# Kernel tuning notes

Measured on AMD Instinct MI355X. Metric: run time of the kernel, lower is better.

Reference implementation:

```python
import jax, jax.numpy as jnp
import numpy as np

B, L = 2, 4096
D_MODEL, STATE, CONV, EXPAND, HEADDIM = 1024, 128, 4, 2, 64
D_INNER = EXPAND * D_MODEL            # 2048
NHEADS = D_INNER // HEADDIM           # 32
CONV_DIM = D_INNER + 2 * STATE        # x, B, C channels (ngroups=1)
D_IN_PROJ = 2 * D_INNER + 2 * STATE + NHEADS
MLP_INNER = 4096
EPS = 1e-5

def _silu(x):
    return x * jax.nn.sigmoid(x)

def _rmsnorm_prenorm(x, res, w):
    # rmsnorm_fn(prenorm=True): residual update then RMSNorm of the residual
    res = x + res
    normed = res * jax.lax.rsqrt(jnp.mean(res * res, axis=-1, keepdims=True) + EPS)
    return normed * w, res

def _mamba2(x, in_proj_w, conv_w, conv_b, dt_bias, A_log, D_param, out_proj_w):
    b, l, _ = x.shape
    zxbcdt = x @ in_proj_w.T                                   # (b,l,D_IN_PROJ)
    z, xBC, dt = jnp.split(zxbcdt, [D_INNER, D_INNER + CONV_DIM], axis=-1)
    # causal depthwise conv1d + silu over [x, B, C]
    xp = jnp.pad(xBC, ((0, 0), (CONV - 1, 0), (0, 0)))
    conv = sum(xp[:, j:j + l, :] * conv_w[None, None, :, j] for j in range(CONV)) + conv_b
    xBC = _silu(conv)
    xh, Bm, Cm = jnp.split(xBC, [D_INNER, D_INNER + STATE], axis=-1)
    xh = xh.reshape(b, l, NHEADS, HEADDIM)                     # (b,l,h,p)
    dt = jax.nn.softplus(dt + dt_bias)                         # (b,l,h)
    A = -jnp.exp(A_log)                                        # (h,)

    def step(state, inp):
        x_t, B_t, C_t, dt_t = inp                              # (b,h,p),(b,n),(b,n),(b,h)
        dA = jnp.exp(dt_t * A)                                 # (b,h)
        state = state * dA[..., None, None] + jnp.einsum('bh,bhp,bn->bhpn', dt_t, x_t, B_t)
        y_t = jnp.einsum('bhpn,bn->bhp', state, C_t)
        return state, y_t

    xs = (xh.transpose(1, 0, 2, 3), Bm.transpose(1, 0, 2), Cm.transpose(1, 0, 2), dt.transpose(1, 0, 2))
    state0 = jnp.zeros((b, NHEADS, HEADDIM, STATE), dtype=x.dtype)
    _, y = jax.lax.scan(step, state0, xs)                      # y: (l,b,h,p)
    y = y.transpose(1, 0, 2, 3) + D_param[None, None, :, None] * xh
    y = y * _silu(z).reshape(b, l, NHEADS, HEADDIM)            # rmsnorm=False -> gate with silu(z)
    return y.reshape(b, l, D_INNER) @ out_proj_w.T

def _mlp(x, gate_w, up_w, down_w):
    return (_silu(x @ gate_w.T) * (x @ up_w.T)) @ down_w.T

def setup_inputs() -> dict:
    key = jax.random.key(0)
    ks = jax.random.split(key, 12)
    s = 0.02
    return {
        'hidden_states': jax.random.normal(ks[0], (B, L, D_MODEL), jnp.float32),
        'residual': jax.random.normal(ks[1], (B, L, D_MODEL), jnp.float32),
        'ssm_norm_w': jnp.ones((D_MODEL,), jnp.float32),
        'mlp_norm_w': jnp.ones((D_MODEL,), jnp.float32),
        'in_proj_w': jax.random.normal(ks[2], (D_IN_PROJ, D_MODEL), jnp.float32) * s,
        'conv_w': jax.random.normal(ks[3], (CONV_DIM, CONV), jnp.float32) * 0.1,
        'conv_b': jnp.zeros((CONV_DIM,), jnp.float32),
        'dt_bias': jax.random.uniform(ks[4], (NHEADS,), jnp.float32, -4.0, -1.0),
        'A_log': jnp.log(jax.random.uniform(ks[5], (NHEADS,), jnp.float32, 1.0, 16.0)),
        'D_param': jnp.ones((NHEADS,), jnp.float32),
        'out_proj_w': jax.random.normal(ks[6], (D_MODEL, D_INNER), jnp.float32) * s,
        'mlp_gate_w': jax.random.normal(ks[7], (MLP_INNER, D_MODEL), jnp.float32) * s,
        'mlp_up_w': jax.random.normal(ks[8], (MLP_INNER, D_MODEL), jnp.float32) * s,
        'mlp_down_w': jax.random.normal(ks[9], (D_MODEL, MLP_INNER), jnp.float32) * s,
    }

def reference(hidden_states, residual, ssm_norm_w, mlp_norm_w, in_proj_w, conv_w, conv_b,
              dt_bias, A_log, D_param, out_proj_w, mlp_gate_w, mlp_up_w, mlp_down_w):
    h, res = _rmsnorm_prenorm(hidden_states, residual, ssm_norm_w)
    h = _mamba2(h, in_proj_w, conv_w, conv_b, dt_bias, A_log, D_param, out_proj_w)
    h, res = _rmsnorm_prenorm(h, res, mlp_norm_w)
    h = _mlp(h, mlp_gate_w, mlp_up_w, mlp_down_w)
    return h, res
```

## Files before the change

### kernel.cpp

```cpp
#include <hip/hip_runtime.h>

typedef __bf16 bf16x8 __attribute__((ext_vector_type(8)));
typedef float  f32x4  __attribute__((ext_vector_type(4)));

#define GLOAD_LDS16(gp, lp) \
  __builtin_amdgcn_global_load_lds((const __attribute__((address_space(1))) void*)(gp), \
                                   (__attribute__((address_space(3))) void*)(lp), 16, 0, 0)

__device__ __forceinline__ unsigned short f2bf(float f) {
  unsigned u = __float_as_uint(f);
  u += 0x7fffu + ((u >> 16) & 1u);
  return (unsigned short)(u >> 16);
}
__device__ __forceinline__ float bf2f(unsigned short h) {
  return __uint_as_float(((unsigned)h) << 16);
}
__device__ __forceinline__ f32x4 splat4(float v) { f32x4 r = {v, v, v, v}; return r; }

__device__ __forceinline__ f32x4 up4(unsigned lo, unsigned hi) {
  f32x4 r;
  r[0] = __uint_as_float(lo << 16); r[1] = __uint_as_float(lo & 0xffff0000u);
  r[2] = __uint_as_float(hi << 16); r[3] = __uint_as_float(hi & 0xffff0000u);
  return r;
}
__device__ __forceinline__ unsigned pk2(float a, float b) {
  return (unsigned)f2bf(a) | ((unsigned)f2bf(b) << 16);
}

__device__ __forceinline__ void store_out(unsigned short* C, size_t idx, float v) {
  C[idx] = f2bf(v);
}
__device__ __forceinline__ void store_out(float* C, size_t idx, float v) {
  C[idx] = v;
}

__global__ __launch_bounds__(256) void rmsnorm1_kernel(
    const float* __restrict__ hid, const float* __restrict__ resin,
    const float* __restrict__ w, float* __restrict__ resout,
    unsigned short* __restrict__ hout)
{
  const int row = blockIdx.x, t = threadIdx.x;
  const size_t base = (size_t)row * 1024;
  float4 h = ((const float4*)(hid + base))[t];
  float4 r = ((const float4*)(resin + base))[t];
  float4 s; s.x = h.x + r.x; s.y = h.y + r.y; s.z = h.z + r.z; s.w = h.w + r.w;
  float ss = s.x*s.x + s.y*s.y + s.z*s.z + s.w*s.w;
  #pragma unroll
  for (int off = 32; off; off >>= 1) ss += __shfl_down(ss, off, 64);
  __shared__ float red[4];
  if ((t & 63) == 0) red[t >> 6] = ss;
  __syncthreads();
  float tot = red[0] + red[1] + red[2] + red[3];
  float sc = rsqrtf(tot * (1.0f/1024.0f) + 1e-5f);
  ((float4*)(resout + base))[t] = s;
  float4 wv = ((const float4*)w)[t];
  ushort4 o = make_ushort4(f2bf(s.x*sc*wv.x), f2bf(s.y*sc*wv.y),
                           f2bf(s.z*sc*wv.z), f2bf(s.w*sc*wv.w));
  ((ushort4*)(hout + base))[t] = o;
}

__global__ __launch_bounds__(256) void rmsnorm2_kernel(
    const unsigned short* __restrict__ mo, const float* __restrict__ res1,
    const float* __restrict__ w, float* __restrict__ res_out,
    unsigned short* __restrict__ h2)
{
  const int row = blockIdx.x, t = threadIdx.x;
  const size_t base = (size_t)row * 1024;
  float4 r = ((const float4*)(res1 + base))[t];
  ushort4 m = ((const ushort4*)(mo + base))[t];
  float4 s; s.x = r.x + bf2f(m.x); s.y = r.y + bf2f(m.y);
            s.z = r.z + bf2f(m.z); s.w = r.w + bf2f(m.w);
  float ss = s.x*s.x + s.y*s.y + s.z*s.z + s.w*s.w;
  #pragma unroll
  for (int off = 32; off; off >>= 1) ss += __shfl_down(ss, off, 64);
  __shared__ float red[4];
  if ((t & 63) == 0) red[t >> 6] = ss;
  __syncthreads();
  float tot = red[0] + red[1] + red[2] + red[3];
  float sc = rsqrtf(tot * (1.0f/1024.0f) + 1e-5f);
  ((float4*)(res_out + base))[t] = s;
  float4 wv = ((const float4*)w)[t];
  ((ushort4*)(h2 + base))[t] = make_ushort4(f2bf(s.x*sc*wv.x), f2bf(s.y*sc*wv.y),
                                            f2bf(s.z*sc*wv.z), f2bf(s.w*sc*wv.w));
}

__global__ __launch_bounds__(256) void cast_w(
    const float* __restrict__ src, unsigned short* __restrict__ dst,
    int rows, int cols, int prows)
{
  size_t i4 = ((size_t)blockIdx.x * 256 + threadIdx.x) * 4;
  size_t total = (size_t)prows * cols;
  if (i4 >= total) return;
  int r = (int)(i4 / cols);
  ushort4 o;
  if (r < rows) {
    float4 v = *(const float4*)(src + i4);
    o = make_ushort4(f2bf(v.x), f2bf(v.y), f2bf(v.z), f2bf(v.w));
  } else {
    o = make_ushort4(0, 0, 0, 0);
  }
  *(ushort4*)(dst + i4) = o;
}

template <typename OutT>
__global__ __launch_bounds__(256) void gemm_bt(
    const unsigned short* __restrict__ A, const unsigned short* __restrict__ W,
    OutT* __restrict__ C, int M, int N, int K, int lda, int ldc)
{
  __shared__ unsigned short As[128 * 32];
  __shared__ unsigned short Bs[128 * 32];
  const int tid = threadIdx.x;
  const int wave = tid >> 6, lane = tid & 63;
  const int m0 = blockIdx.y << 7, n0 = blockIdx.x << 7;
  const int lr = lane >> 2;
  const int lk = (lane & 3) << 3;
  const int wm = (wave >> 1) << 6, wn = (wave & 1) << 6;
  const int fr = lane & 15, fq = lane >> 4;

  f32x4 acc[4][4];
  #pragma unroll
  for (int i = 0; i < 4; i++)
    #pragma unroll
    for (int j = 0; j < 4; j++)
      #pragma unroll
      for (int r = 0; r < 4; r++) acc[i][j][r] = 0.0f;

  const unsigned short* Abase = A + (size_t)(m0 + wave*32 + lr) * lda + lk;
  const unsigned short* Wbase = W + (size_t)(n0 + wave*32 + lr) * K + lk;
  const size_t rstepA = (size_t)16 * lda;
  const size_t rstepW = (size_t)16 * K;
  unsigned short* AsW = As + (wave*32) * 32;
  unsigned short* BsW = Bs + (wave*32) * 32;

  for (int k0 = 0; k0 < K; k0 += 32) {
    GLOAD_LDS16(Abase + k0,          AsW);
    GLOAD_LDS16(Abase + k0 + rstepA, AsW + 16*32);
    GLOAD_LDS16(Wbase + k0,          BsW);
    GLOAD_LDS16(Wbase + k0 + rstepW, BsW + 16*32);
    __syncthreads();
    bf16x8 af[4], bfv[4];
    #pragma unroll
    for (int i = 0; i < 4; i++) {
      af[i]  = *(const bf16x8*)(As + (wm + i*16 + fr) * 32 + fq*8);
      bfv[i] = *(const bf16x8*)(Bs + (wn + i*16 + fr) * 32 + fq*8);
    }
    #pragma unroll
    for (int i = 0; i < 4; i++)
      #pragma unroll
      for (int j = 0; j < 4; j++)
        acc[i][j] = __builtin_amdgcn_mfma_f32_16x16x32_bf16(af[i], bfv[j], acc[i][j], 0, 0, 0);
    __syncthreads();
  }

  #pragma unroll
  for (int i = 0; i < 4; i++)
    #pragma unroll
    for (int j = 0; j < 4; j++)
      #pragma unroll
      for (int r = 0; r < 4; r++) {
        int gm = m0 + wm + i*16 + fq*4 + r;
        int gn = n0 + wn + j*16 + fr;
        store_out(C, (size_t)gm * ldc + gn, acc[i][j][r]);
      }
}

__global__ __launch_bounds__(256) void conv_dt_kernel(
    const unsigned short* __restrict__ zx, const float* __restrict__ conv_w,
    const float* __restrict__ conv_b, const float* __restrict__ dt_bias,
    const float* __restrict__ A_log, unsigned short* __restrict__ conv_out,
    float2* __restrict__ dtda)
{
  size_t idx = (size_t)blockIdx.x * 256 + threadIdx.x;
  if (idx >= (size_t)8192 * 2336) return;
  int c = (int)(idx % 2336);
  int row = (int)(idx / 2336);
  int l = row & 4095;
  if (c < 2304) {
    float acc = conv_b[c];
    const float* wp = conv_w + c * 4;
    #pragma unroll
    for (int j = 0; j < 4; j++) {
      int ls = l - 3 + j;
      if (ls >= 0) acc += bf2f(zx[(size_t)(row - 3 + j) * 4480 + 2048 + c]) * wp[j];
    }
    float s = acc / (1.0f + expf(-acc));
    conv_out[(size_t)row * 2304 + c] = f2bf(s);
  } else {
    int h = c - 2304;
    float draw = bf2f(zx[(size_t)row * 4480 + 4352 + h]) + dt_bias[h];
    float sp = (draw > 20.0f) ? draw : log1pf(expf(draw));
    float Ah = -expf(A_log[h]);
    dtda[(size_t)row * 32 + h] = make_float2(sp, expf(sp * Ah));
  }
}


__global__ __launch_bounds__(256) void chunk_state_kernel(
    const unsigned short* __restrict__ convo, const float2* __restrict__ dtda,
    const float* __restrict__ A_log, unsigned short* __restrict__ Sg,
    float* __restrict__ Pend)
{
  __shared__ __align__(16) unsigned short bT[128 * 136];
  __shared__ __align__(16) unsigned short xT[64 * 136];
  __shared__ float wsh[128];
  const int t = threadIdx.x, lane = t & 63, wv = t >> 6;
  const int c = blockIdx.x & 31, h = (blockIdx.x >> 5) & 31, b = (int)(blockIdx.x >> 10);
  const size_t r0 = (size_t)b * 4096 + (size_t)c * 128;

  if (wv == 0) {
    const float A = -expf(A_log[h]);
    const float s0 = dtda[(r0 + 2 * lane) * 32 + h].x;
    const float s1 = dtda[(r0 + 2 * lane + 1) * 32 + h].x;
    const float v1 = s1 * A;
    float ps = s0 * A + v1;
    #pragma unroll
    for (int off = 1; off < 64; off <<= 1) {
      float n = __shfl_up(ps, off, 64);
      if (lane >= off) ps += n;
    }
    const float laQ = __shfl(ps, 63, 64);
    wsh[2 * lane]     = expf(laQ - (ps - v1)) * s0;
    wsh[2 * lane + 1] = expf(laQ - ps) * s1;
    if (lane == 63) Pend[blockIdx.x] = expf(laQ);
  }
  __syncthreads();

  {
    int j = t >> 3;
    const int p0 = (t & 7) << 3;
    #pragma unroll
    for (int it = 0; it < 4; ++it, j += 32) {
      const uint4 v = *(const uint4*)(convo + (r0 + j) * 2304 + h * 64 + p0);
      const float w = wsh[j];
      const unsigned arr[4] = {v.x, v.y, v.z, v.w};
      #pragma unroll
      for (int e = 0; e < 8; ++e) {
        const unsigned short raw = (unsigned short)(arr[e >> 1] >> ((e & 1) * 16));
        xT[(p0 + e) * 136 + j] = f2bf(bf2f(raw) * w);
      }
    }
  }
  {
    int j = t >> 4;
    const int n0 = (t & 15) << 3;
    #pragma unroll
    for (int it = 0; it < 8; ++it, j += 16) {
      const uint4 v = *(const uint4*)(convo + (r0 + j) * 2304 + 2048 + n0);
      const unsigned arr[4] = {v.x, v.y, v.z, v.w};
      #pragma unroll
      for (int e = 0; e < 8; ++e)
        bT[(n0 + e) * 136 + j] = (unsigned short)(arr[e >> 1] >> ((e & 1) * 16));
    }
  }
  __syncthreads();

  const int fr = lane & 15, fq = lane >> 4;
  const int wn = wv << 5;
  f32x4 acc[4][2];
  #pragma unroll
  for (int i = 0; i < 4; ++i)
    #pragma unroll
    for (int j = 0; j < 2; ++j) acc[i][j] = splat4(0.f);

  #pragma unroll
  for (int k0 = 0; k0 < 128; k0 += 32) {
    bf16x8 af[4], bf[2];
    #pragma unroll
    for (int i = 0; i < 4; ++i)
      af[i] = *(const bf16x8*)(xT + (i * 16 + fr) * 136 + fq * 8 + k0);
    #pragma unroll
    for (int j = 0; j < 2; ++j)
      bf[j] = *(const bf16x8*)(bT + (wn + j * 16 + fr) * 136 + fq * 8 + k0);
    #pragma unroll
    for (int i = 0; i < 4; ++i)
      #pragma unroll
      for (int j = 0; j < 2; ++j)
        acc[i][j] = __builtin_amdgcn_mfma_f32_16x16x32_bf16(af[i], bf[j], acc[i][j], 0, 0, 0);
  }

  const size_t slot = (size_t)blockIdx.x * 8192;
  #pragma unroll
  for (int i = 0; i < 4; ++i)
    #pragma unroll
    for (int j = 0; j < 2; ++j)
      #pragma unroll
      for (int r = 0; r < 4; ++r)
        Sg[slot + (size_t)(i * 16 + fq * 4 + r) * 128 + wn + j * 16 + fr] = f2bf(acc[i][j][r]);
}

__global__ __launch_bounds__(256) void chunk_combine_kernel(
    unsigned short* __restrict__ S, const float* __restrict__ Pend)
{
  const int t = threadIdx.x;
  const int sl = blockIdx.x & 7, bh = blockIdx.x >> 3;
  const size_t e = (size_t)sl * 1024 + (size_t)t * 4;
  f32x4 run = splat4(0.f);
  for (int c = 0; c < 32; ++c) {
    const size_t addr = (size_t)(bh * 32 + c) * 8192 + e;
    const uint2 a = *(const uint2*)(S + addr);
    const float P = Pend[bh * 32 + c];
    *(uint2*)(S + addr) = make_uint2(pk2(run[0], run[1]), pk2(run[2], run[3]));
    const f32x4 av = up4(a.x, a.y);
    run = av + splat4(P) * run;
  }
}

__global__ __launch_bounds__(256, 2) void chunk_output_kernel(
    unsigned short* __restrict__ convo, const float2* __restrict__ dtda,
    const float* __restrict__ A_log, const unsigned short* __restrict__ Sg,
    const unsigned short* __restrict__ zx, const float* __restrict__ D_param)
{
  __shared__ __align__(16) unsigned short bm[128 * 136];
  __shared__ __align__(16) unsigned short xT[64 * 136];
  __shared__ float la_s[128];
  __shared__ float dt_s[128];
  const int t = threadIdx.x, lane = t & 63, wv = t >> 6;
  const int c = blockIdx.x & 31, h = (blockIdx.x >> 5) & 31, b = (int)(blockIdx.x >> 10);
  const size_t r0 = (size_t)b * 4096 + (size_t)c * 128;

  if (wv == 0) {
    const float A = -expf(A_log[h]);
    const float s0 = dtda[(r0 + 2 * lane) * 32 + h].x;
    const float s1 = dtda[(r0 + 2 * lane + 1) * 32 + h].x;
    const float v1 = s1 * A;
    float ps = s0 * A + v1;
    #pragma unroll
    for (int off = 1; off < 64; off <<= 1) {
      float n = __shfl_up(ps, off, 64);
      if (lane >= off) ps += n;
    }
    la_s[2 * lane] = ps - v1;
    la_s[2 * lane + 1] = ps;
    dt_s[2 * lane] = s0;
    dt_s[2 * lane + 1] = s1;
  }

  {
    int j = t >> 4;
    const int n0 = (t & 15) << 3;
    #pragma unroll
    for (int it = 0; it < 8; ++it, j += 16)
      *(uint4*)(bm + j * 136 + n0) = *(const uint4*)(convo + (r0 + j) * 2304 + 2048 + n0);
  }
  {
    int j = t >> 3;
    const int p0 = (t & 7) << 3;
    #pragma unroll
    for (int it = 0; it < 4; ++it, j += 32) {
      const uint4 v = *(const uint4*)(convo + (r0 + j) * 2304 + h * 64 + p0);
      const unsigned arr[4] = {v.x, v.y, v.z, v.w};
      #pragma unroll
      for (int e = 0; e < 8; ++e)
        xT[(p0 + e) * 136 + j] = (unsigned short)(arr[e >> 1] >> ((e & 1) * 16));
    }
  }
  __syncthreads();

  const int fr = lane & 15, fq = lane >> 4;
  const int wm = wv << 5;
  const unsigned short* Cbase = convo + r0 * 2304 + 2176 + fq * 8;

  f32x4 acc_g[2][8];
  #pragma unroll
  for (int mt = 0; mt < 2; ++mt)
    #pragma unroll
    for (int nt = 0; nt < 8; ++nt) acc_g[mt][nt] = splat4(0.f);
  #pragma unroll
  for (int k0 = 0; k0 < 128; k0 += 32) {
    bf16x8 af[2], bg[8];
    #pragma unroll
    for (int mt = 0; mt < 2; ++mt)
      af[mt] = *(const bf16x8*)(Cbase + (size_t)(wm + mt * 16 + fr) * 2304 + k0);
    #pragma unroll
    for (int nt = 0; nt < 8; ++nt)
      bg[nt] = *(const bf16x8*)(bm + (nt * 16 + fr) * 136 + fq * 8 + k0);
    #pragma unroll
    for (int mt = 0; mt < 2; ++mt)
      #pragma unroll
      for (int nt = 0; nt < 8; ++nt)
        acc_g[mt][nt] = __builtin_amdgcn_mfma_f32_16x16x32_bf16(af[mt], bg[nt], acc_g[mt][nt], 0, 0, 0);
  }
  __syncthreads();

  #pragma unroll
  for (int mt = 0; mt < 2; ++mt)
    #pragma unroll
    for (int r = 0; r < 4; ++r) {
      const int i = wm + mt * 16 + fq * 4 + r;
      const float lai = la_s[i];
      #pragma unroll
      for (int nt = 0; nt < 8; ++nt) {
        const int j = nt * 16 + fr;
        float v = 0.f;
        if (j <= i) v = acc_g[mt][nt][r] * expf(lai - la_s[j]) * dt_s[j];
        bm[i * 136 + j] = f2bf(v);
      }
    }

  const size_t slot = (size_t)blockIdx.x * 8192;
  f32x4 acc_y[2][4];
  #pragma unroll
  for (int mt = 0; mt < 2; ++mt)
    #pragma unroll
    for (int pt = 0; pt < 4; ++pt) acc_y[mt][pt] = splat4(0.f);
  #pragma unroll
  for (int k0 = 0; k0 < 128; k0 += 32) {
    bf16x8 af[2], bs[4];
    #pragma unroll
    for (int mt = 0; mt < 2; ++mt)
      af[mt] = *(const bf16x8*)(Cbase + (size_t)(wm + mt * 16 + fr) * 2304 + k0);
    #pragma unroll
    for (int pt = 0; pt < 4; ++pt)
      bs[pt] = *(const bf16x8*)(Sg + slot + (size_t)(pt * 16 + fr) * 128 + fq * 8 + k0);
    #pragma unroll
    for (int mt = 0; mt < 2; ++mt)
      #pragma unroll
      for (int pt = 0; pt < 4; ++pt)
        acc_y[mt][pt] = __builtin_amdgcn_mfma_f32_16x16x32_bf16(af[mt], bs[pt], acc_y[mt][pt], 0, 0, 0);
  }
  #pragma unroll
  for (int mt = 0; mt < 2; ++mt)
    #pragma unroll
    for (int r = 0; r < 4; ++r) {
      const float el = expf(la_s[wm + mt * 16 + fq * 4 + r]);
      #pragma unroll
      for (int pt = 0; pt < 4; ++pt) acc_y[mt][pt][r] *= el;
    }
  __syncthreads();

  #pragma unroll
  for (int k0 = 0; k0 < 128; k0 += 32) {
    bf16x8 am[2], bx[4];
    #pragma unroll
    for (int mt = 0; mt < 2; ++mt)
      am[mt] = *(const bf16x8*)(bm + (wm + mt * 16 + fr) * 136 + fq * 8 + k0);
    #pragma unroll
    for (int pt = 0; pt < 4; ++pt)
      bx[pt] = *(const bf16x8*)(xT + (pt * 16 + fr) * 136 + fq * 8 + k0);
    #pragma unroll
    for (int mt = 0; mt < 2; ++mt)
      #pragma unroll
      for (int pt = 0; pt < 4; ++pt)
        acc_y[mt][pt] = __builtin_amdgcn_mfma_f32_16x16x32_bf16(am[mt], bx[pt], acc_y[mt][pt], 0, 0, 0);
  }

  const float D = D_param[h];
  #pragma unroll
  for (int mt = 0; mt < 2; ++mt)
    #pragma unroll
    for (int r = 0; r < 4; ++r) {
      const int i = wm + mt * 16 + fq * 4 + r;
      const size_t grow = r0 + i;
      #pragma unroll
      for (int pt = 0; pt < 4; ++pt) {
        const int p = pt * 16 + fr;
        const float x = bf2f(xT[p * 136 + i]);
        const float z = bf2f(zx[grow * 4480 + h * 64 + p]);
        const float sg = z / (1.0f + expf(-z));
        convo[grow * 2304 + h * 64 + p] = f2bf((acc_y[mt][pt][r] + D * x) * sg);
      }
    }
}

__global__ __launch_bounds__(256) void act_kernel(
    unsigned short* __restrict__ g, const unsigned short* __restrict__ u)
{
  size_t i4 = ((size_t)blockIdx.x * 256 + threadIdx.x) * 4;
  if (i4 >= (size_t)8192 * 4096) return;
  ushort4 gv = *(ushort4*)(g + i4);
  ushort4 uv = *(const ushort4*)(u + i4);
  float x, s, o[4];
  x = bf2f(gv.x); s = x / (1.0f + expf(-x)); o[0] = s * bf2f(uv.x);
  x = bf2f(gv.y); s = x / (1.0f + expf(-x)); o[1] = s * bf2f(uv.y);
  x = bf2f(gv.z); s = x / (1.0f + expf(-x)); o[2] = s * bf2f(uv.z);
  x = bf2f(gv.w); s = x / (1.0f + expf(-x)); o[3] = s * bf2f(uv.w);
  *(ushort4*)(g + i4) = make_ushort4(f2bf(o[0]), f2bf(o[1]), f2bf(o[2]), f2bf(o[3]));
}

static constexpr size_t OFF_RES1 = 0;
static constexpr size_t OFF_H1   = 33554432;
static constexpr size_t OFF_W    = 83886080;
static constexpr size_t OFF_ZX   = 93061120;
static constexpr size_t OFF_CONV = 166461440;
static constexpr size_t OFF_DTDA = 204210176;
static constexpr size_t OFF_U    = 0;

extern "C" void kernel_launch(void* const* d_in, const int* in_sizes, int n_in,
                              void* d_out, int out_size, void* d_ws, size_t ws_size,
                              hipStream_t stream) {
  const float* hid      = (const float*)d_in[0];
  const float* resid    = (const float*)d_in[1];
  const float* ssm_w    = (const float*)d_in[2];
  const float* mlp_w    = (const float*)d_in[3];
  const float* in_proj  = (const float*)d_in[4];
  const float* conv_w   = (const float*)d_in[5];
  const float* conv_b   = (const float*)d_in[6];
  const float* dt_bias  = (const float*)d_in[7];
  const float* A_log    = (const float*)d_in[8];
  const float* D_param  = (const float*)d_in[9];
  const float* out_proj = (const float*)d_in[10];
  const float* gate_w   = (const float*)d_in[11];
  const float* up_w     = (const float*)d_in[12];
  const float* down_w   = (const float*)d_in[13];
  float* out = (float*)d_out;
  char* ws = (char*)d_ws;

  float*          res1  = (float*)(ws + OFF_RES1);
  unsigned short* h1    = (unsigned short*)(ws + OFF_H1);
  unsigned short* Wb    = (unsigned short*)(ws + OFF_W);
  unsigned short* zx    = (unsigned short*)(ws + OFF_ZX);
  unsigned short* convo = (unsigned short*)(ws + OFF_CONV);
  float2*         dtda  = (float2*)(ws + OFF_DTDA);
  unsigned short* ub    = (unsigned short*)(ws + OFF_U);
  unsigned short* Sg    = h1;
  float*          Pend  = (float*)(ws + OFF_W);

  rmsnorm1_kernel<<<8192, 256, 0, stream>>>(hid, resid, ssm_w, res1, h1);
  cast_w<<<4480, 256, 0, stream>>>(in_proj, Wb, 4384, 1024, 4480);
  gemm_bt<unsigned short><<<dim3(35, 64), 256, 0, stream>>>(h1, Wb, zx, 8192, 4480, 1024, 1024, 4480);
  conv_dt_kernel<<<74752, 256, 0, stream>>>(zx, conv_w, conv_b, dt_bias, A_log,
                                            convo, dtda);
  chunk_state_kernel<<<2048, 256, 0, stream>>>(convo, dtda, A_log, Sg, Pend);
  chunk_combine_kernel<<<512, 256, 0, stream>>>(Sg, Pend);
  chunk_output_kernel<<<2048, 256, 0, stream>>>(convo, dtda, A_log, Sg, zx, D_param);
  cast_w<<<2048, 256, 0, stream>>>(out_proj, Wb, 1024, 2048, 1024);
  gemm_bt<unsigned short><<<dim3(8, 64), 256, 0, stream>>>(convo, Wb, h1, 8192, 1024, 2048, 2304, 1024);
  rmsnorm2_kernel<<<8192, 256, 0, stream>>>(h1, res1, mlp_w, out + 8388608, convo);
  cast_w<<<4096, 256, 0, stream>>>(gate_w, Wb, 4096, 1024, 4096);
  gemm_bt<unsigned short><<<dim3(32, 64), 256, 0, stream>>>(convo, Wb, zx, 8192, 4096, 1024, 1024, 4096);
  cast_w<<<4096, 256, 0, stream>>>(up_w, Wb, 4096, 1024, 4096);
  gemm_bt<unsigned short><<<dim3(32, 64), 256, 0, stream>>>(convo, Wb, ub, 8192, 4096, 1024, 1024, 4096);
  act_kernel<<<32768, 256, 0, stream>>>(zx, ub);
  cast_w<<<4096, 256, 0, stream>>>(down_w, Wb, 1024, 4096, 1024);
  gemm_bt<float><<<dim3(8, 64), 256, 0, stream>>>(zx, Wb, out, 8192, 1024, 4096, 4096, 1024);
}
```

Measured before the change: 891.9 us.

## Replace GEMM with 256x256 double-buffered swizzled-LDS kernel and XCD remapping

```diff
diff --git a/kernel.cpp b/kernel.cpp
--- a/kernel.cpp
+++ b/kernel.cpp
@@ -103,64 +103,109 @@
 }
 
 template <typename OutT>
-__global__ __launch_bounds__(256) void gemm_bt(
+__global__ __launch_bounds__(512) void gemm256(
     const unsigned short* __restrict__ A, const unsigned short* __restrict__ W,
-    OutT* __restrict__ C, int M, int N, int K, int lda, int ldc)
-{
-  __shared__ unsigned short As[128 * 32];
-  __shared__ unsigned short Bs[128 * 32];
-  const int tid = threadIdx.x;
-  const int wave = tid >> 6, lane = tid & 63;
-  const int m0 = blockIdx.y << 7, n0 = blockIdx.x << 7;
-  const int lr = lane >> 2;
-  const int lk = (lane & 3) << 3;
-  const int wm = (wave >> 1) << 6, wn = (wave & 1) << 6;
+    OutT* __restrict__ C, int K, int lda, int ldc, int Nst)
+{
+  __shared__ unsigned short As[2][2][8192];
+  __shared__ unsigned short Bs[2][2][8192];
+
+  const int gx = gridDim.x, nwg = gx * (int)gridDim.y;
+  int lin = blockIdx.y * gx + blockIdx.x;
+  {
+    const int q = nwg >> 3, r = nwg & 7, xcd = lin & 7, lo = lin >> 3;
+    lin = (xcd < r ? xcd * (q + 1) : r * (q + 1) + (xcd - r) * q) + lo;
+  }
+  const int n0 = (lin % gx) << 8, m0 = (lin / gx) << 8;
+
+  const int t = threadIdx.x, lane = t & 63, w = t >> 6;
+  const int wr = w >> 2, wc = w & 3;
   const int fr = lane & 15, fq = lane >> 4;
-
-  f32x4 acc[4][4];
-  #pragma unroll
-  for (int i = 0; i < 4; i++)
-    #pragma unroll
-    for (int j = 0; j < 4; j++)
-      #pragma unroll
-      for (int r = 0; r < 4; r++) acc[i][j][r] = 0.0f;
-
-  const unsigned short* Abase = A + (size_t)(m0 + wave*32 + lr) * lda + lk;
-  const unsigned short* Wbase = W + (size_t)(n0 + wave*32 + lr) * K + lk;
-  const size_t rstepA = (size_t)16 * lda;
-  const size_t rstepW = (size_t)16 * K;
-  unsigned short* AsW = As + (wave*32) * 32;
-  unsigned short* BsW = Bs + (wave*32) * 32;
-
-  for (int k0 = 0; k0 < K; k0 += 32) {
-    GLOAD_LDS16(Abase + k0,          AsW);
-    GLOAD_LDS16(Abase + k0 + rstepA, AsW + 16*32);
-    GLOAD_LDS16(Wbase + k0,          BsW);
-    GLOAD_LDS16(Wbase + k0 + rstepW, BsW + 16*32);
-    __syncthreads();
-    bf16x8 af[4], bfv[4];
-    #pragma unroll
-    for (int i = 0; i < 4; i++) {
-      af[i]  = *(const bf16x8*)(As + (wm + i*16 + fr) * 32 + fq*8);
-      bfv[i] = *(const bf16x8*)(Bs + (wn + i*16 + fr) * 32 + fq*8);
-    }
-    #pragma unroll
-    for (int i = 0; i < 4; i++)
-      #pragma unroll
-      for (int j = 0; j < 4; j++)
-        acc[i][j] = __builtin_amdgcn_mfma_f32_16x16x32_bf16(af[i], bfv[j], acc[i][j], 0, 0, 0);
-    __syncthreads();
-  }
-
-  #pragma unroll
-  for (int i = 0; i < 4; i++)
-    #pragma unroll
-    for (int j = 0; j < 4; j++)
-      #pragma unroll
-      for (int r = 0; r < 4; r++) {
-        int gm = m0 + wm + i*16 + fq*4 + r;
-        int gn = n0 + wn + j*16 + fr;
-        store_out(C, (size_t)gm * ldc + gn, acc[i][j][r]);
+  const int l3 = lane >> 3;
+  const int sc = ((lane & 7) ^ l3) << 3;
+  const int sr = (w << 3) + l3;
+  const int cswz = (fr & 7) << 3;
+  const int brow0 = (wc & 1) << 6;
+
+  f32x4 acc[8][4];
+  #pragma unroll
+  for (int i = 0; i < 8; ++i)
+    #pragma unroll
+    for (int j = 0; j < 4; ++j) acc[i][j] = splat4(0.f);
+
+  auto stageA = [&](int buf, int h, int kc) {
+    const unsigned short* g = A + (size_t)(m0 + h * 128 + sr) * lda + kc + sc;
+    GLOAD_LDS16(g,                    &As[buf][h][w << 9]);
+    GLOAD_LDS16(g + (size_t)64 * lda, &As[buf][h][4096 + (w << 9)]);
+  };
+  auto stageB = [&](int buf, int h, int kc) {
+    const unsigned short* g = W + (size_t)(n0 + h * 128 + sr) * (size_t)K + kc + sc;
+    GLOAD_LDS16(g,                  &Bs[buf][h][w << 9]);
+    GLOAD_LDS16(g + (size_t)64 * K, &Bs[buf][h][4096 + (w << 9)]);
+  };
+
+#define QUAD(CB, MG, NG)                                                        \
+  do {                                                                          \
+    const unsigned short* Ah = &As[(CB)][wr][0];                                \
+    const unsigned short* Bh = &Bs[(CB)][wc >> 1][0];                           \
+    bf16x8 af[4][2], bq[2][2];                                                  \
+    _Pragma("unroll") for (int m2 = 0; m2 < 4; ++m2)                            \
+      _Pragma("unroll") for (int ks = 0; ks < 2; ++ks)                          \
+        af[m2][ks] = *(const bf16x8*)(Ah + ((MG)*64 + m2*16 + fr) * 64          \
+                                        + ((ks*32 + fq*8) ^ cswz));             \
+    _Pragma("unroll") for (int n2 = 0; n2 < 2; ++n2)                            \
+      _Pragma("unroll") for (int ks = 0; ks < 2; ++ks)                          \
+        bq[n2][ks] = *(const bf16x8*)(Bh + (brow0 + (NG)*32 + n2*16 + fr) * 64  \
+                                        + ((ks*32 + fq*8) ^ cswz));             \
+    asm volatile("s_waitcnt lgkmcnt(0)" ::: "memory");                          \
+    __builtin_amdgcn_sched_barrier(0);                                          \
+    __builtin_amdgcn_s_setprio(1);                                              \
+    _Pragma("unroll") for (int ks = 0; ks < 2; ++ks)                            \
+      _Pragma("unroll") for (int m2 = 0; m2 < 4; ++m2)                          \
+        _Pragma("unroll") for (int n2 = 0; n2 < 2; ++n2)                        \
+          acc[(MG)*4 + m2][(NG)*2 + n2] = __builtin_amdgcn_mfma_f32_16x16x32_bf16( \
+              af[m2][ks], bq[n2][ks], acc[(MG)*4 + m2][(NG)*2 + n2], 0, 0, 0);  \
+    __builtin_amdgcn_s_setprio(0);                                              \
+  } while (0)
+
+  stageA(0, 0, 0); stageA(0, 1, 0);
+  stageB(0, 0, 0); stageB(0, 1, 0);
+
+  const int NKT = K >> 6;
+  for (int kt = 0; kt < NKT; ++kt) {
+    const int cb = kt & 1, nb = cb ^ 1;
+    const bool pre = (kt + 1 < NKT);
+    const int kc = (kt + 1) << 6;
+    if (pre) {
+      stageA(nb, 0, kc);
+      asm volatile("s_waitcnt vmcnt(2)" ::: "memory");
+    } else {
+      asm volatile("s_waitcnt vmcnt(0)" ::: "memory");
+    }
+    __builtin_amdgcn_s_barrier();
+    QUAD(cb, 0, 0);
+    __builtin_amdgcn_s_barrier();
+    if (pre) stageA(nb, 1, kc);
+    QUAD(cb, 1, 0);
+    __builtin_amdgcn_s_barrier();
+    if (pre) stageB(nb, 0, kc);
+    QUAD(cb, 0, 1);
+    __builtin_amdgcn_s_barrier();
+    if (pre) stageB(nb, 1, kc);
+    QUAD(cb, 1, 1);
+    __builtin_amdgcn_s_barrier();
+  }
+#undef QUAD
+
+  #pragma unroll
+  for (int mi = 0; mi < 8; ++mi)
+    #pragma unroll
+    for (int ni = 0; ni < 4; ++ni)
+      #pragma unroll
+      for (int rr = 0; rr < 4; ++rr) {
+        const int gm = m0 + wr * 128 + mi * 16 + fq * 4 + rr;
+        const int gn = n0 + wc * 64 + ni * 16 + fr;
+        if (gn < Nst) store_out(C, (size_t)gm * ldc + gn, acc[mi][ni][rr]);
       }
 }
 
@@ -514,23 +559,24 @@
   unsigned short* ub    = (unsigned short*)(ws + OFF_U);
   unsigned short* Sg    = h1;
   float*          Pend  = (float*)(ws + OFF_W);
+  unsigned short* WinP  = convo;
 
   rmsnorm1_kernel<<<8192, 256, 0, stream>>>(hid, resid, ssm_w, res1, h1);
-  cast_w<<<4480, 256, 0, stream>>>(in_proj, Wb, 4384, 1024, 4480);
-  gemm_bt<unsigned short><<<dim3(35, 64), 256, 0, stream>>>(h1, Wb, zx, 8192, 4480, 1024, 1024, 4480);
+  cast_w<<<4608, 256, 0, stream>>>(in_proj, WinP, 4384, 1024, 4608);
+  gemm256<unsigned short><<<dim3(18, 32), 512, 0, stream>>>(h1, WinP, zx, 1024, 1024, 4480, 4480);
   conv_dt_kernel<<<74752, 256, 0, stream>>>(zx, conv_w, conv_b, dt_bias, A_log,
                                             convo, dtda);
   chunk_state_kernel<<<2048, 256, 0, stream>>>(convo, dtda, A_log, Sg, Pend);
   chunk_combine_kernel<<<512, 256, 0, stream>>>(Sg, Pend);
   chunk_output_kernel<<<2048, 256, 0, stream>>>(convo, dtda, A_log, Sg, zx, D_param);
   cast_w<<<2048, 256, 0, stream>>>(out_proj, Wb, 1024, 2048, 1024);
-  gemm_bt<unsigned short><<<dim3(8, 64), 256, 0, stream>>>(convo, Wb, h1, 8192, 1024, 2048, 2304, 1024);
+  gemm256<unsigned short><<<dim3(4, 32), 512, 0, stream>>>(convo, Wb, h1, 2048, 2304, 1024, 1024);
   rmsnorm2_kernel<<<8192, 256, 0, stream>>>(h1, res1, mlp_w, out + 8388608, convo);
   cast_w<<<4096, 256, 0, stream>>>(gate_w, Wb, 4096, 1024, 4096);
-  gemm_bt<unsigned short><<<dim3(32, 64), 256, 0, stream>>>(convo, Wb, zx, 8192, 4096, 1024, 1024, 4096);
+  gemm256<unsigned short><<<dim3(16, 32), 512, 0, stream>>>(convo, Wb, zx, 1024, 1024, 4096, 4096);
   cast_w<<<4096, 256, 0, stream>>>(up_w, Wb, 4096, 1024, 4096);
-  gemm_bt<unsigned short><<<dim3(32, 64), 256, 0, stream>>>(convo, Wb, ub, 8192, 4096, 1024, 1024, 4096);
+  gemm256<unsigned short><<<dim3(16, 32), 512, 0, stream>>>(convo, Wb, ub, 1024, 1024, 4096, 4096);
   act_kernel<<<32768, 256, 0, stream>>>(zx, ub);
   cast_w<<<4096, 256, 0, stream>>>(down_w, Wb, 1024, 4096, 1024);
-  gemm_bt<float><<<dim3(8, 64), 256, 0, stream>>>(zx, Wb, out, 8192, 1024, 4096, 4096, 1024);
-}
+  gemm256<float><<<dim3(4, 32), 512, 0, stream>>>(zx, Wb, out, 4096, 4096, 1024, 1024);
+}
```

New measurement: 1.096 ms. 1.23x slower.
